# Kernel optimization log

Hardware: AMD Instinct MI355X
Metric: run time of the kernel (lower is better)

Reference implementation:

```python
import jax, jax.numpy as jnp
import numpy as np

B, N, DF = 8, 4096, 768
K1, K2, DS = 8, 2, 128
KVQ, H, ITERS = 128, 1, 3
DH = KVQ // H
EPS_SA = 1e-8
SCALE = DH ** -0.5


def layer_norm(x, g, b, eps=1e-5):
    m = jnp.mean(x, axis=-1, keepdims=True)
    v = jnp.var(x, axis=-1, keepdims=True)
    return (x - m) / jnp.sqrt(v + eps) * g + b


def gru_cell(x, h, Wih, Whh, bih, bhh):
    gi = x @ Wih.T + bih
    gh = h @ Whh.T + bhh
    ir, iz, inn = jnp.split(gi, 3, axis=-1)
    hr, hz, hn = jnp.split(gh, 3, axis=-1)
    r = jax.nn.sigmoid(ir + hr)
    z = jax.nn.sigmoid(iz + hz)
    n = jnp.tanh(inn + r * hn)
    return (1.0 - z) * n + z * h


def setup_inputs() -> dict:
    key = jax.random.key(0)
    ks = jax.random.split(key, 24)
    s = 0.02
    f32 = jnp.float32
    return {
        'tokens': jax.random.normal(ks[0], (B, N, DF), f32),
        'parent_slots': jax.random.normal(ks[1], (B, K1, DS), f32),
        'parent_masks': jax.random.uniform(ks[2], (B, K1, N), f32),
        'eps_noise': jax.random.normal(ks[3], (B, K1, K2, DS), f32),
        'ln_in_g': jnp.ones((DF,), f32), 'ln_in_b': jnp.zeros((DF,), f32),
        'ln_s_g': jnp.ones((DS,), f32), 'ln_s_b': jnp.zeros((DS,), f32),
        'Wq': jax.random.normal(ks[4], (KVQ, DS), f32) * s,
        'Wk': jax.random.normal(ks[5], (KVQ, DF), f32) * s,
        'Wv': jax.random.normal(ks[6], (KVQ, DF), f32) * s,
        'gru_Wih': jax.random.normal(ks[7], (3 * DS, KVQ), f32) * s,
        'gru_Whh': jax.random.normal(ks[8], (3 * DS, DS), f32) * s,
        'gru_bih': jnp.zeros((3 * DS,), f32),
        'gru_bhh': jnp.zeros((3 * DS,), f32),
        'mlp_ln_g': jnp.ones((DS,), f32), 'mlp_ln_b': jnp.zeros((DS,), f32),
        'mlp_W1': jax.random.normal(ks[9], (4 * DS, DS), f32) * s,
        'mlp_b1': jnp.zeros((4 * DS,), f32),
        'mlp_W2': jax.random.normal(ks[10], (DS, 4 * DS), f32) * s,
        'mlp_b2': jnp.zeros((DS,), f32),
    }


def reference(tokens, parent_slots, parent_masks, eps_noise,
              ln_in_g, ln_in_b, ln_s_g, ln_s_b, Wq, Wk, Wv,
              gru_Wih, gru_Whh, gru_bih, gru_bhh,
              mlp_ln_g, mlp_ln_b, mlp_W1, mlp_b1, mlp_W2, mlp_b2):
    BK = B * K1
    # parent-mask gating (all parents vectorized, folded into batch)
    denom = jnp.mean(parent_masks, axis=-1, keepdims=True)          # [B,K1,1]
    safe = (denom > 1e-6).astype(tokens.dtype)
    w_scaled = safe * (parent_masks / (denom + 1e-6)) + (1.0 - safe)  # [B,K1,N]
    tg = (tokens[:, None, :, :] * w_scaled[..., None]).reshape(BK, N, DF)
    slots = (parent_slots[:, :, None, :] + 0.01 * eps_noise).reshape(BK, K2, DS)

    inp = layer_norm(tg, ln_in_g, ln_in_b)
    k = (inp @ Wk.T).reshape(BK, N, H, DH)
    v = (inp @ Wv.T).reshape(BK, N, H, DH)

    attn_bw = None
    for _ in range(ITERS):
        slots_prev = slots
        sn = layer_norm(slots, ln_s_g, ln_s_b)
        q = (sn @ Wq.T).reshape(BK, K2, H, DH)
        dots = jnp.einsum('bihd,bjhd->bihj', q, k) * SCALE          # [BK,K2,H,N]
        attn = jax.nn.softmax(dots, axis=1) + EPS_SA                # softmax over slots
        attn_bw = attn
        attn_w = attn / jnp.sum(attn, axis=-1, keepdims=True)
        updates = jnp.einsum('bjhd,bihj->bihd', v, attn_w).reshape(BK * K2, KVQ)
        slots = gru_cell(updates, slots_prev.reshape(BK * K2, DS),
                         gru_Wih, gru_Whh, gru_bih, gru_bhh).reshape(BK, K2, DS)
        h = layer_norm(slots, mlp_ln_g, mlp_ln_b)
        slots = jax.nn.gelu(h @ mlp_W1.T + mlp_b1, approximate=False) @ mlp_W2.T + mlp_b2

    attn_out = jnp.mean(attn_bw, axis=2)                            # [BK,K2,N]
    child_objects = slots.reshape(B, K1 * K2, DS)
    child_gating = (attn_out.reshape(B, K1, K2, N) * parent_masks[:, :, None, :]).reshape(B, K1 * K2, N)
    return child_objects, child_gating
```

## Files before the change

### kernel.cpp

```cpp
#include <hip/hip_runtime.h>
#include <math.h>

#define SCALE_ 0.08838834764831843f

typedef __attribute__((ext_vector_type(8))) short bf16x8;
typedef __attribute__((ext_vector_type(4))) float f32x4;
typedef __attribute__((ext_vector_type(8))) unsigned short u16x8;

static const size_t OFF_VAR   = 0;
static const size_t OFF_DENOM = 32768;
static const size_t OFF_GSUM  = 32832;
static const size_t OFF_BIAS  = 33088;
static const size_t OFF_QKB   = 33344;
static const size_t OFF_SSUM  = 33472;
static const size_t OFF_SLOTS = 33600;
static const size_t OFF_Q     = 49984;
static const size_t OFF_WQBF  = 66368;
static const size_t OFF_WIHBF = 74560;
static const size_t OFF_WHHBF = 99136;
static const size_t OFF_W1BF  = 123712;
static const size_t OFF_WM2BF = 156480;
static const size_t OFF_WKVBF = 189248;
static const size_t OFF_UPART = 287552;
static const size_t OFF_KVB   = 811840;

__device__ __forceinline__ float wred64(float v) {
#pragma unroll
  for (int off = 32; off > 0; off >>= 1) v += __shfl_xor(v, off, 64);
  return v;
}

__device__ __forceinline__ unsigned short f2bf(float f) {
  unsigned u = __float_as_uint(f);
  unsigned r = (u + 0x7fffu + ((u >> 16) & 1u)) >> 16;
  return (unsigned short)r;
}

__device__ __forceinline__ unsigned pack2(float a, float b) {
  return (unsigned)f2bf(a) | ((unsigned)f2bf(b) << 16);
}

__device__ __forceinline__ float bf2f(unsigned short s) {
  return __uint_as_float((unsigned)s << 16);
}

__global__ __launch_bounds__(256) void prep_all_k(
    const float* __restrict__ Wk, const float* __restrict__ Wv,
    const float* __restrict__ g, const float* __restrict__ bb,
    const float* __restrict__ Wq, const float* __restrict__ Wih,
    const float* __restrict__ Whh, const float* __restrict__ W1,
    const float* __restrict__ W2, const float* __restrict__ pm,
    unsigned short* __restrict__ wkv, float* __restrict__ gsum,
    float* __restrict__ biasArr,
    unsigned short* __restrict__ Wqbf, unsigned short* __restrict__ Wihbf,
    unsigned short* __restrict__ Whhbf, unsigned short* __restrict__ W1bf,
    unsigned short* __restrict__ Wm2bf, float* __restrict__ denomArr)
{
  __shared__ float red4[4];
  int bi = blockIdx.x, t = threadIdx.x;
  if (bi < 64) {
    int j = bi*4 + (t >> 6), lane = t & 63;
    const float* w = (j < 128) ? (Wk + (size_t)j*768) : (Wv + (size_t)(j-128)*768);
    float gs = 0.f, bs = 0.f;
#pragma unroll
    for (int s = 0; s < 12; ++s) {
      int dd = lane + s*64;
      float wv = w[dd], gv = g[dd];
      gs += gv*wv; bs += bb[dd]*wv;
      wkv[(size_t)j*768 + dd] = f2bf(wv*gv);
    }
    gs = wred64(gs); bs = wred64(bs);
    if (lane == 0) { gsum[j] = gs; biasArr[j] = bs; }
  } else if (bi < 128) {
    int idx = (bi-64)*256 + t;  Wqbf[idx]  = f2bf(Wq[idx]);
  } else if (bi < 320) {
    int idx = (bi-128)*256 + t; Wihbf[idx] = f2bf(Wih[idx]);
  } else if (bi < 512) {
    int idx = (bi-320)*256 + t; Whhbf[idx] = f2bf(Whh[idx]);
  } else if (bi < 768) {
    int idx = (bi-512)*256 + t; W1bf[idx]  = f2bf(W1[idx]);
  } else if (bi < 1024) {
    int idx = (bi-768)*256 + t; Wm2bf[idx] = f2bf(W2[idx]);
  } else {
    int bk = bi - 1024;
    float s = 0.f;
#pragma unroll
    for (int k = 0; k < 16; ++k) s += pm[bk*4096 + t + k*256];
    s = wred64(s);
    if ((t & 63) == 0) red4[t >> 6] = s;
    __syncthreads();
    if (t == 0) denomArr[bk] = (red4[0]+red4[1]+red4[2]+red4[3])*(1.f/4096.f);
  }
}

#define DMA_B(kstep, buf) \
  { int k0_ = (kstep)*32; \
    _Pragma("unroll") \
    for (int s_ = 0; s_ < 4; ++s_) { \
      int nb_ = w*64 + s_*16; \
      __builtin_amdgcn_global_load_lds( \
        (const __attribute__((address_space(1))) void*) \
          (wkv + (size_t)(nb_ + nrow)*768 + k0_ + gsw*8), \
        (__attribute__((address_space(3))) void*)(Bs + (buf)*8192 + nb_*32), \
        16, 0, 0); \
    } }

__global__ __launch_bounds__(256) void gemm_kv_k(
    const float* __restrict__ tokens, const unsigned short* __restrict__ wkv,
    const float* __restrict__ gsum, unsigned short* __restrict__ KVb,
    float* __restrict__ varArr)
{
  __shared__ unsigned short Bs[2*8192];
  int r0 = blockIdx.x*64;
  int t = threadIdx.x;
  int w = t >> 6, lane = t & 63;
  int lm = lane & 15, lq = lane >> 4;
  int nrow = lane >> 2;
  int gsw = (lane & 3) ^ ((lane >> 3) & 3);
  int nswz = lq ^ ((lm >> 1) & 3);

  const float* aptr = tokens + (size_t)(r0 + w*16 + lm)*768 + lq*8;

  f32x4 acc[16];
#pragma unroll
  for (int c = 0; c < 16; ++c) acc[c] = f32x4{0.f, 0.f, 0.f, 0.f};
  float s1 = 0.f, s2 = 0.f;

  float4 A0[2], A1[2];
  DMA_B(0, 0);
  A0[0] = *(const float4*)(aptr);
  A1[0] = *(const float4*)(aptr + 4);
  DMA_B(1, 1);
  __builtin_amdgcn_s_waitcnt(0x0F76);
  __builtin_amdgcn_s_barrier();

#pragma unroll
  for (int k = 0; k < 24; ++k) {
    const int kb = k & 1, kn = kb ^ 1;
    float4 x0 = A0[kb], x1 = A1[kb];
    s1 += x0.x + x0.y + x0.z + x0.w + x1.x + x1.y + x1.z + x1.w;
    s2 += x0.x*x0.x + x0.y*x0.y + x0.z*x0.z + x0.w*x0.w
        + x1.x*x1.x + x1.y*x1.y + x1.z*x1.z + x1.w*x1.w;
    unsigned u0 = pack2(x0.x, x0.y), u1 = pack2(x0.z, x0.w);
    unsigned u2 = pack2(x1.x, x1.y), u3 = pack2(x1.z, x1.w);
    bf16x8 afrag;
    { uint4 tmp = make_uint4(u0, u1, u2, u3);
      afrag = *(bf16x8*)&tmp; }
    if (k < 23) {
      A0[kn] = *(const float4*)(aptr + (k+1)*32);
      A1[kn] = *(const float4*)(aptr + (k+1)*32 + 4);
    }
    const unsigned short* bsr = Bs + kb*8192;
#pragma unroll
    for (int nt = 0; nt < 16; ++nt) {
      bf16x8 bfr = *(const bf16x8*)(bsr + (nt*16 + lm)*32 + nswz*8);
      acc[nt] = __builtin_amdgcn_mfma_f32_16x16x32_bf16(afrag, bfr, acc[nt], 0, 0, 0);
    }
    if (k < 23) {
      __builtin_amdgcn_s_barrier();
      if (k < 22) {
        DMA_B(k+2, kb);
        __builtin_amdgcn_s_waitcnt(0x0F76);
      } else {
        __builtin_amdgcn_s_waitcnt(0x0F72);
      }
      __builtin_amdgcn_s_barrier();
    }
  }

  s1 += __shfl_xor(s1, 16, 64); s1 += __shfl_xor(s1, 32, 64);
  s2 += __shfl_xor(s2, 16, 64); s2 += __shfl_xor(s2, 32, 64);
  float mean = s1*(1.f/768.f);
  float var  = s2*(1.f/768.f) - mean*mean;
  if (lq == 0) varArr[r0 + w*16 + lm] = var;
  float meanR[4];
#pragma unroll
  for (int reg = 0; reg < 4; ++reg)
    meanR[reg] = __shfl(mean, lq*4 + reg, 64);
#pragma unroll
  for (int nt = 0; nt < 16; ++nt) {
    int col = nt*16 + lm;
    float gs = gsum[col];
#pragma unroll
    for (int reg = 0; reg < 4; ++reg) {
      int row = r0 + w*16 + lq*4 + reg;
      KVb[(size_t)row*256 + col] = f2bf(acc[nt][reg] - meanR[reg]*gs);
    }
  }
}

__global__ __launch_bounds__(256, 1) void slots_init_q_k(
    const float* __restrict__ ps, const float* __restrict__ eps,
    const float* __restrict__ g_s, const float* __restrict__ b_s,
    const unsigned short* __restrict__ Wqbf, const float* __restrict__ biasArr,
    float* __restrict__ slots, float* __restrict__ qg, float* __restrict__ qkb,
    float* __restrict__ Ssum)
{
  __shared__ unsigned short Fsn[2048];
  __shared__ float qkbL[16];
  int R0 = blockIdx.x*16;
  int t = threadIdx.x;
  int w = t >> 6, ln = t & 63, lm = ln & 15, lq = ln >> 4;
  if (t < 16) qkbL[t] = 0.f;
  {
    int r = t >> 4, dseg = t & 15, ds8 = dseg*8;
    int row = R0 + r, bk = row >> 1;
    float xv[8]; float s1 = 0.f, s2 = 0.f;
#pragma unroll
    for (int j = 0; j < 8; ++j) {
      int d = ds8 + j;
      float x = ps[bk*128 + d] + 0.01f*eps[row*128 + d];
      slots[row*128 + d] = x;
      xv[j] = x; s1 += x; s2 += x*x;
    }
#pragma unroll
    for (int m = 8; m >= 1; m >>= 1) {
      s1 += __shfl_xor(s1, m, 16);
      s2 += __shfl_xor(s2, m, 16);
    }
    float mean = s1*(1.f/128.f);
    float var = s2*(1.f/128.f) - mean*mean;
    float rstd = rsqrtf(var + 1e-5f);
    float sv[8];
#pragma unroll
    for (int j = 0; j < 8; ++j) {
      int d = ds8 + j;
      sv[j] = (xv[j] - mean)*rstd*g_s[d] + b_s[d];
    }
    int fa = ((dseg >> 2)*64 + (dseg & 3)*16 + r)*8;
    *(uint4*)&Fsn[fa] = make_uint4(pack2(sv[0],sv[1]), pack2(sv[2],sv[3]),
                                   pack2(sv[4],sv[5]), pack2(sv[6],sv[7]));
  }
  __syncthreads();
  {
    bf16x8 af[4];
#pragma unroll
    for (int kc = 0; kc < 4; ++kc)
      af[kc] = *(const bf16x8*)(&Fsn[(kc*64 + ln)*8]);
    float pr[4] = {0.f, 0.f, 0.f, 0.f};
#pragma unroll
    for (int i = 0; i < 2; ++i) {
      int n0 = w*32 + i*16;
      f32x4 acc = f32x4{0.f,0.f,0.f,0.f};
#pragma unroll
      for (int kc = 0; kc < 4; ++kc) {
        bf16x8 bw = *(const bf16x8*)(&Wqbf[(size_t)(n0+lm)*128 + kc*32 + lq*8]);
        acc = __builtin_amdgcn_mfma_f32_16x16x32_bf16(af[kc], bw, acc, 0,0,0);
      }
      int n = n0 + lm;
      float bk_ = biasArr[n];
#pragma unroll
      for (int reg = 0; reg < 4; ++reg) {
        int row = lq*4 + reg;
        qg[(size_t)(R0 + row)*128 + n] = acc[reg];
        pr[reg] += acc[reg]*bk_;
      }
    }
#pragma unroll
    for (int reg = 0; reg < 4; ++reg) {
#pragma unroll
      for (int m = 8; m >= 1; m >>= 1) pr[reg] += __shfl_xor(pr[reg], m, 16);
    }
    if (lm == 0) {
#pragma unroll
      for (int reg = 0; reg < 4; ++reg)
        atomicAdd(&qkbL[lq*4 + reg], pr[reg]);
    }
  }
  __syncthreads();
  if (t < 16) { qkb[R0 + t] = qkbL[t]; Ssum[R0 + t] = 0.f; }
}

__global__ __launch_bounds__(256) void attn_fused_k(
    const unsigned short* __restrict__ KVb, const float* __restrict__ qg,
    const float* __restrict__ qkb, const float* __restrict__ varArr,
    const float* __restrict__ denomArr, const float* __restrict__ pm,
    float* __restrict__ Upart, float* __restrict__ Ssum,
    float* __restrict__ outG, int last)
{
  __shared__ float KVs[32*260];
  __shared__ float qs[2048];
  __shared__ float was[16*33];
  __shared__ float qkbs[16];
  int bi = blockIdx.x;
  int b = bi & 7, ch = bi >> 3;
  int t = threadIdx.x;
#pragma unroll
  for (int s = 0; s < 2; ++s)
    ((float4*)qs)[s*256 + t] = ((const float4*)(qg + b*2048))[s*256 + t];
  if (t < 16) qkbs[t] = qkb[b*16 + t];
  int p = t >> 5, nl = t & 31;
  int iu = t >> 4, dg = t & 15;
  int bk = b*8 + p;
  float den = denomArr[bk];
  float acc8[8];
#pragma unroll
  for (int j = 0; j < 8; ++j) acc8[j] = 0.f;
  float sA0 = 0.f, sA1 = 0.f;
  const float* q0 = qs + (p*2)*128;
  const float* q1 = q0 + 128;
  __syncthreads();
  float qb0 = qkbs[p*2], qb1 = qkbs[p*2 + 1];
  for (int sub = 0; sub < 4; ++sub) {
    int n0 = ch*128 + sub*32;
    if (sub) __syncthreads();
    {
      int nn = t >> 3, jj = t & 7;
#pragma unroll
      for (int s = 0; s < 4; ++s) {
        int col8 = jj + s*8;
        u16x8 kv8 = *(const u16x8*)&KVb[((size_t)(b*4096 + n0 + nn))*256 + col8*8];
        float4 f0, f1;
        f0.x = bf2f(kv8[0]); f0.y = bf2f(kv8[1]); f0.z = bf2f(kv8[2]); f0.w = bf2f(kv8[3]);
        f1.x = bf2f(kv8[4]); f1.y = bf2f(kv8[5]); f1.z = bf2f(kv8[6]); f1.w = bf2f(kv8[7]);
        *(float4*)&KVs[nn*260 + col8*8] = f0;
        *(float4*)&KVs[nn*260 + col8*8 + 4] = f1;
      }
    }
    __syncthreads();
    float d0 = 0.f, d1 = 0.f;
    const float* kr = KVs + nl*260;
#pragma unroll 8
    for (int j4 = 0; j4 < 32; ++j4) {
      float4 kv = *(const float4*)(kr + j4*4);
      float4 qa = *(const float4*)(q0 + j4*4);
      float4 qb = *(const float4*)(q1 + j4*4);
      d0 += kv.x*qa.x + kv.y*qa.y + kv.z*qa.z + kv.w*qa.w;
      d1 += kv.x*qb.x + kv.y*qb.y + kv.z*qb.z + kv.w*qb.w;
    }
    int n = n0 + nl;
    float pmv = pm[(size_t)bk*4096 + n];
    float c = (den > 1e-6f) ? (pmv/(den + 1e-6f)) : 1.f;
    float vv = varArr[b*4096 + n];
    float al = c*rsqrtf(c*c*vv + 1e-5f);
    float dd0 = SCALE_*(al*d0 + qb0);
    float dd1 = SCALE_*(al*d1 + qb1);
    float mx = fmaxf(dd0, dd1);
    float e0 = expf(dd0 - mx), e1 = expf(dd1 - mx);
    float inv = 1.f/(e0 + e1);
    float o0 = e0*inv + 1e-8f;
    float o1 = e1*inv + 1e-8f;
    sA0 += o0; sA1 += o1;
    was[(p*2)*33 + nl] = o0*al;
    was[(p*2 + 1)*33 + nl] = o1*al;
    if (last) {
      outG[((size_t)(bk*2))*4096 + n] = o0*pmv;
      outG[((size_t)(bk*2 + 1))*4096 + n] = o1*pmv;
    }
    __syncthreads();
    const float* vb = KVs + 128 + dg*8;
    const float* wr = was + iu*33;
#pragma unroll 8
    for (int nn = 0; nn < 32; ++nn) {
      float wv = wr[nn];
      float4 v0 = *(const float4*)(vb + nn*260);
      float4 v1 = *(const float4*)(vb + nn*260 + 4);
      acc8[0] += wv*v0.x; acc8[1] += wv*v0.y; acc8[2] += wv*v0.z; acc8[3] += wv*v0.w;
      acc8[4] += wv*v1.x; acc8[5] += wv*v1.y; acc8[6] += wv*v1.z; acc8[7] += wv*v1.w;
    }
  }
#pragma unroll
  for (int m = 16; m >= 1; m >>= 1) {
    sA0 += __shfl_xor(sA0, m, 32);
    sA1 += __shfl_xor(sA1, m, 32);
  }
  if (nl == 0) {
    atomicAdd(&Ssum[bk*2], sA0);
    atomicAdd(&Ssum[bk*2 + 1], sA1);
  }
  float* up = Upart + ((size_t)(bi*16 + iu))*128 + dg*8;
  *(float4*)up = make_float4(acc8[0], acc8[1], acc8[2], acc8[3]);
  *(float4*)(up + 4) = make_float4(acc8[4], acc8[5], acc8[6], acc8[7]);
}

__global__ __launch_bounds__(256, 1) void gru_mlp_q_k(
    const float* __restrict__ Upart, const float* __restrict__ Ssum,
    const float* __restrict__ biasArr,
    const unsigned short* __restrict__ Wihbf, const unsigned short* __restrict__ Whhbf,
    const float* __restrict__ bih, const float* __restrict__ bhh,
    const float* __restrict__ mlp_g, const float* __restrict__ mlp_b,
    const unsigned short* __restrict__ W1bf, const float* __restrict__ b1,
    const unsigned short* __restrict__ Wm2bf, const float* __restrict__ b2,
    const float* __restrict__ ln_s_g, const float* __restrict__ ln_s_b,
    const unsigned short* __restrict__ Wqbf,
    float* __restrict__ slots, float* __restrict__ qg, float* __restrict__ qkb,
    float* __restrict__ SsumW, float* __restrict__ outObj, int last)
{
  __shared__ unsigned short FXx[2048], FXh[2048], Fhn[2048], Fsn[2048];
  __shared__ unsigned short Ft1[8192];
  __shared__ float G_rz[16*256];
  __shared__ float G_in[16*128];
  __shared__ float G_hn[16*128];
  __shared__ float hs_[16*128];
  __shared__ float os_[16*128];
  __shared__ float qkbL[16];

  int R0 = blockIdx.x*16;
  int t = threadIdx.x;
  int w = t >> 6, ln = t & 63;
  int lm = ln & 15, lq = ln >> 4;

  {
    int r = t >> 4, dseg = t & 15, ds8 = dseg*8;
    int R = R0 + r;
    float ua[8];
#pragma unroll
    for (int j = 0; j < 8; ++j) ua[j] = 0.f;
    const float* up = Upart + (size_t)R*128 + ds8;
#pragma unroll
    for (int ch = 0; ch < 32; ++ch) {
      float4 u0 = *(const float4*)(up + (size_t)ch*16384);
      float4 u1 = *(const float4*)(up + (size_t)ch*16384 + 4);
      ua[0]+=u0.x; ua[1]+=u0.y; ua[2]+=u0.z; ua[3]+=u0.w;
      ua[4]+=u1.x; ua[5]+=u1.y; ua[6]+=u1.z; ua[7]+=u1.w;
    }
    float Sv = 1.f/Ssum[R];
    float4 bv0 = *(const float4*)(biasArr + 128 + ds8);
    float4 bv1 = *(const float4*)(biasArr + 132 + ds8);
    float xv[8];
    xv[0]=ua[0]*Sv+bv0.x; xv[1]=ua[1]*Sv+bv0.y; xv[2]=ua[2]*Sv+bv0.z; xv[3]=ua[3]*Sv+bv0.w;
    xv[4]=ua[4]*Sv+bv1.x; xv[5]=ua[5]*Sv+bv1.y; xv[6]=ua[6]*Sv+bv1.z; xv[7]=ua[7]*Sv+bv1.w;
    float4 h0 = *(const float4*)(slots + (size_t)R*128 + ds8);
    float4 h1 = *(const float4*)(slots + (size_t)R*128 + ds8 + 4);
    *(float4*)(hs_ + r*128 + ds8) = h0;
    *(float4*)(hs_ + r*128 + ds8 + 4) = h1;
    int fa = ((dseg >> 2)*64 + (dseg & 3)*16 + r)*8;
    *(uint4*)&FXx[fa] = make_uint4(pack2(xv[0],xv[1]), pack2(xv[2],xv[3]),
                                   pack2(xv[4],xv[5]), pack2(xv[6],xv[7]));
    *(uint4*)&FXh[fa] = make_uint4(pack2(h0.x,h0.y), pack2(h0.z,h0.w),
                                   pack2(h1.x,h1.y), pack2(h1.z,h1.w));
    if (t < 16) qkbL[t] = 0.f;
  }
  __syncthreads();

  {
    bf16x8 ax[4], ah[4];
#pragma unroll
    for (int kc = 0; kc < 4; ++kc) {
      ax[kc] = *(const bf16x8*)(&FXx[(kc*64 + ln)*8]);
      ah[kc] = *(const bf16x8*)(&FXh[(kc*64 + ln)*8]);
    }
    if (w < 2) {
#pragma unroll
      for (int i = 0; i < 8; ++i) {
        int n0 = (w*8 + i)*16;
        f32x4 acc = f32x4{0.f,0.f,0.f,0.f};
#pragma unroll
        for (int kc = 0; kc < 4; ++kc) {
          bf16x8 bi_ = *(const bf16x8*)(&Wihbf[(size_t)(n0+lm)*128 + kc*32 + lq*8]);
          acc = __builtin_amdgcn_mfma_f32_16x16x32_bf16(ax[kc], bi_, acc, 0,0,0);
        }
#pragma unroll
        for (int kc = 0; kc < 4; ++kc) {
          bf16x8 bh_ = *(const bf16x8*)(&Whhbf[(size_t)(n0+lm)*128 + kc*32 + lq*8]);
          acc = __builtin_amdgcn_mfma_f32_16x16x32_bf16(ah[kc], bh_, acc, 0,0,0);
        }
#pragma unroll
        for (int reg = 0; reg < 4; ++reg)
          G_rz[(lq*4+reg)*256 + n0 + lm] = acc[reg];
      }
    } else if (w == 2) {
#pragma unroll
      for (int i = 0; i < 8; ++i) {
        int n0 = 256 + i*16;
        f32x4 acc = f32x4{0.f,0.f,0.f,0.f};
#pragma unroll
        for (int kc = 0; kc < 4; ++kc) {
          bf16x8 bi_ = *(const bf16x8*)(&Wihbf[(size_t)(n0+lm)*128 + kc*32 + lq*8]);
          acc = __builtin_amdgcn_mfma_f32_16x16x32_bf16(ax[kc], bi_, acc, 0,0,0);
        }
#pragma unroll
        for (int reg = 0; reg < 4; ++reg)
          G_in[(lq*4+reg)*128 + i*16 + lm] = acc[reg];
      }
    } else {
#pragma unroll
      for (int i = 0; i < 8; ++i) {
        int n0 = 256 + i*16;
        f32x4 acc = f32x4{0.f,0.f,0.f,0.f};
#pragma unroll
        for (int kc = 0; kc < 4; ++kc) {
          bf16x8 bh_ = *(const bf16x8*)(&Whhbf[(size_t)(n0+lm)*128 + kc*32 + lq*8]);
          acc = __builtin_amdgcn_mfma_f32_16x16x32_bf16(ah[kc], bh_, acc, 0,0,0);
        }
#pragma unroll
        for (int reg = 0; reg < 4; ++reg)
          G_hn[(lq*4+reg)*128 + i*16 + lm] = acc[reg];
      }
    }
  }
  __syncthreads();

  {
    int r = t >> 4, dseg = t & 15, ds8 = dseg*8;
    float hp[8];
    float s1 = 0.f, s2 = 0.f;
#pragma unroll
    for (int j = 0; j < 8; ++j) {
      int d = ds8 + j;
      float rg = G_rz[r*256 + d] + bih[d] + bhh[d];
      float zg = G_rz[r*256 + 128 + d] + bih[128+d] + bhh[128+d];
      float ing = G_in[r*128 + d] + bih[256+d];
      float hng = G_hn[r*128 + d] + bhh[256+d];
      float rv = 1.f/(1.f + expf(-rg));
      float zv = 1.f/(1.f + expf(-zg));
      float nv = tanhf(ing + rv*hng);
      float h0 = hs_[r*128 + d];
      float h = (1.f - zv)*nv + zv*h0;
      hp[j] = h;
      s1 += h; s2 += h*h;
    }
#pragma unroll
    for (int m = 8; m >= 1; m >>= 1) {
      s1 += __shfl_xor(s1, m, 16);
      s2 += __shfl_xor(s2, m, 16);
    }
    float mean = s1*(1.f/128.f);
    float var = s2*(1.f/128.f) - mean*mean;
    float rstd = rsqrtf(var + 1e-5f);
    float hv[8];
#pragma unroll
    for (int j = 0; j < 8; ++j) {
      int d = ds8 + j;
      hv[j] = (hp[j] - mean)*rstd*mlp_g[d] + mlp_b[d];
    }
    int fa = ((dseg >> 2)*64 + (dseg & 3)*16 + r)*8;
    *(uint4*)&Fhn[fa] = make_uint4(pack2(hv[0],hv[1]), pack2(hv[2],hv[3]),
                                   pack2(hv[4],hv[5]), pack2(hv[6],hv[7]));
  }
  __syncthreads();

  {
    bf16x8 af[4];
#pragma unroll
    for (int kc = 0; kc < 4; ++kc)
      af[kc] = *(const bf16x8*)(&Fhn[(kc*64 + ln)*8]);
#pragma unroll
    for (int i = 0; i < 8; ++i) {
      int n0 = (w*8 + i)*16;
      f32x4 acc = f32x4{0.f,0.f,0.f,0.f};
#pragma unroll
      for (int kc = 0; kc < 4; ++kc) {
        bf16x8 bw = *(const bf16x8*)(&W1bf[(size_t)(n0+lm)*128 + kc*32 + lq*8]);
        acc = __builtin_amdgcn_mfma_f32_16x16x32_bf16(af[kc], bw, acc, 0,0,0);
      }
      int kdim = n0 + lm;
      float bb = b1[kdim];
      int kc2 = kdim >> 5;
      int sub = (kdim >> 3) & 3;
      int jj = kdim & 7;
#pragma unroll
      for (int reg = 0; reg < 4; ++reg) {
        float v = acc[reg] + bb;
        float gel = 0.5f*v*(1.f + erff(v*0.70710678118654752f));
        Ft1[(kc2*64 + sub*16 + lq*4 + reg)*8 + jj] = f2bf(gel);
      }
    }
  }
  __syncthreads();

  {
#pragma unroll
    for (int i = 0; i < 2; ++i) {
      int n0 = w*32 + i*16;
      f32x4 acc = f32x4{0.f,0.f,0.f,0.f};
#pragma unroll
      for (int kc = 0; kc < 16; ++kc) {
        bf16x8 af = *(const bf16x8*)(&Ft1[(kc*64 + ln)*8]);
        bf16x8 bw = *(const bf16x8*)(&Wm2bf[(size_t)(n0+lm)*512 + kc*32 + lq*8]);
        acc = __builtin_amdgcn_mfma_f32_16x16x32_bf16(af, bw, acc, 0,0,0);
      }
      int n = n0 + lm;
      float bb = b2[n];
#pragma unroll
      for (int reg = 0; reg < 4; ++reg) {
        int row = lq*4 + reg;
        float o = acc[reg] + bb;
        slots[(size_t)(R0 + row)*128 + n] = o;
        os_[row*128 + n] = o;
        if (last) outObj[(size_t)(R0 + row)*128 + n] = o;
      }
    }
  }

  if (last) return;

  __syncthreads();
  {
    int r = t >> 4, dseg = t & 15, ds8 = dseg*8;
    float ov[8];
    float s1 = 0.f, s2 = 0.f;
#pragma unroll
    for (int j = 0; j < 8; ++j) {
      float o = os_[r*128 + ds8 + j];
      ov[j] = o; s1 += o; s2 += o*o;
    }
#pragma unroll
    for (int m = 8; m >= 1; m >>= 1) {
      s1 += __shfl_xor(s1, m, 16);
      s2 += __shfl_xor(s2, m, 16);
    }
    float mean = s1*(1.f/128.f);
    float var = s2*(1.f/128.f) - mean*mean;
    float rstd = rsqrtf(var + 1e-5f);
    float sv[8];
#pragma unroll
    for (int j = 0; j < 8; ++j) {
      int d = ds8 + j;
      sv[j] = (ov[j] - mean)*rstd*ln_s_g[d] + ln_s_b[d];
    }
    int fa = ((dseg >> 2)*64 + (dseg & 3)*16 + r)*8;
    *(uint4*)&Fsn[fa] = make_uint4(pack2(sv[0],sv[1]), pack2(sv[2],sv[3]),
                                   pack2(sv[4],sv[5]), pack2(sv[6],sv[7]));
  }
  __syncthreads();

  {
    bf16x8 af[4];
#pragma unroll
    for (int kc = 0; kc < 4; ++kc)
      af[kc] = *(const bf16x8*)(&Fsn[(kc*64 + ln)*8]);
    float pr[4] = {0.f, 0.f, 0.f, 0.f};
#pragma unroll
    for (int i = 0; i < 2; ++i) {
      int n0 = w*32 + i*16;
      f32x4 acc = f32x4{0.f,0.f,0.f,0.f};
#pragma unroll
      for (int kc = 0; kc < 4; ++kc) {
        bf16x8 bw = *(const bf16x8*)(&Wqbf[(size_t)(n0+lm)*128 + kc*32 + lq*8]);
        acc = __builtin_amdgcn_mfma_f32_16x16x32_bf16(af[kc], bw, acc, 0,0,0);
      }
      int n = n0 + lm;
      float bk_ = biasArr[n];
#pragma unroll
      for (int reg = 0; reg < 4; ++reg) {
        int row = lq*4 + reg;
        qg[(size_t)(R0 + row)*128 + n] = acc[reg];
        pr[reg] += acc[reg]*bk_;
      }
    }
#pragma unroll
    for (int reg = 0; reg < 4; ++reg) {
#pragma unroll
      for (int m = 8; m >= 1; m >>= 1) pr[reg] += __shfl_xor(pr[reg], m, 16);
    }
    if (lm == 0) {
#pragma unroll
      for (int reg = 0; reg < 4; ++reg)
        atomicAdd(&qkbL[lq*4 + reg], pr[reg]);
    }
  }
  __syncthreads();
  if (t < 16) {
    qkb[R0 + t] = qkbL[t];
    SsumW[R0 + t] = 0.f;
  }
}

extern "C" void kernel_launch(void* const* d_in, const int* in_sizes, int n_in,
                              void* d_out, int out_size, void* d_ws, size_t ws_size,
                              hipStream_t stream) {
  const float* tokens = (const float*)d_in[0];
  const float* pslots = (const float*)d_in[1];
  const float* pmasks = (const float*)d_in[2];
  const float* eps    = (const float*)d_in[3];
  const float* ln_in_g= (const float*)d_in[4];
  const float* ln_in_b= (const float*)d_in[5];
  const float* ln_s_g = (const float*)d_in[6];
  const float* ln_s_b = (const float*)d_in[7];
  const float* Wq     = (const float*)d_in[8];
  const float* Wk     = (const float*)d_in[9];
  const float* Wv     = (const float*)d_in[10];
  const float* Wih    = (const float*)d_in[11];
  const float* Whh    = (const float*)d_in[12];
  const float* bih    = (const float*)d_in[13];
  const float* bhh    = (const float*)d_in[14];
  const float* mlp_g  = (const float*)d_in[15];
  const float* mlp_b  = (const float*)d_in[16];
  const float* W1     = (const float*)d_in[17];
  const float* b1     = (const float*)d_in[18];
  const float* W2     = (const float*)d_in[19];
  const float* b2     = (const float*)d_in[20];
  float* ws  = (float*)d_ws;
  float* out = (float*)d_out;
  unsigned short* wkvbf = (unsigned short*)(ws + OFF_WKVBF);
  unsigned short* wqbf  = (unsigned short*)(ws + OFF_WQBF);
  unsigned short* wihbf = (unsigned short*)(ws + OFF_WIHBF);
  unsigned short* whhbf = (unsigned short*)(ws + OFF_WHHBF);
  unsigned short* w1bf  = (unsigned short*)(ws + OFF_W1BF);
  unsigned short* wm2bf = (unsigned short*)(ws + OFF_WM2BF);
  unsigned short* kvb   = (unsigned short*)(ws + OFF_KVB);

  prep_all_k<<<1088, 256, 0, stream>>>(Wk, Wv, ln_in_g, ln_in_b,
                                       Wq, Wih, Whh, W1, W2, pmasks,
                                       wkvbf, ws + OFF_GSUM, ws + OFF_BIAS,
                                       wqbf, wihbf, whhbf, w1bf, wm2bf,
                                       ws + OFF_DENOM);
  gemm_kv_k<<<512, 256, 0, stream>>>(tokens, wkvbf, ws + OFF_GSUM,
                                     kvb, ws + OFF_VAR);
  slots_init_q_k<<<8, 256, 0, stream>>>(pslots, eps, ln_s_g, ln_s_b,
                                        wqbf, ws + OFF_BIAS,
                                        ws + OFF_SLOTS, ws + OFF_Q,
                                        ws + OFF_QKB, ws + OFF_SSUM);
  for (int it = 0; it < 3; ++it) {
    int last = (it == 2);
    attn_fused_k<<<256, 256, 0, stream>>>(kvb, ws + OFF_Q, ws + OFF_QKB,
                                          ws + OFF_VAR, ws + OFF_DENOM, pmasks,
                                          ws + OFF_UPART, ws + OFF_SSUM,
                                          out + 16384, last);
    gru_mlp_q_k<<<8, 256, 0, stream>>>(ws + OFF_UPART, ws + OFF_SSUM,
                                       ws + OFF_BIAS, wihbf, whhbf, bih, bhh,
                                       mlp_g, mlp_b, w1bf, b1, wm2bf, b2,
                                       ln_s_g, ln_s_b, wqbf,
                                       ws + OFF_SLOTS, ws + OFF_Q, ws + OFF_QKB,
                                       ws + OFF_SSUM, out, last);
  }
}
```

Measured before the change: 380.3 us.

## Use MFMA for attention dots and updates with split K and transposed V layout

The attention kernel now computes q·k dots and the weighted V sum with bf16 MFMA instructions instead of scalar FP32 loops over LDS-staged K/V. To support this, the KV projection GEMM writes K row-major and V transposed per batch, and it loads B fragments straight from global memory into registers instead of using an LDS DMA double buffer. Each block now covers a 128-token chunk of one batch with two waves, which doubles the number of partial update buffers that the GRU kernel has to reduce. Rounding the softmax weights to bf16 adds precision loss, and the strided transposed V stores in the GEMM may cost extra write bandwidth.

```diff
diff --git a/kernel.cpp b/kernel.cpp
--- a/kernel.cpp
+++ b/kernel.cpp
@@ -5,7 +5,6 @@
 
 typedef __attribute__((ext_vector_type(8))) short bf16x8;
 typedef __attribute__((ext_vector_type(4))) float f32x4;
-typedef __attribute__((ext_vector_type(8))) unsigned short u16x8;
 
 static const size_t OFF_VAR   = 0;
 static const size_t OFF_DENOM = 32768;
@@ -22,7 +21,8 @@
 static const size_t OFF_WM2BF = 156480;
 static const size_t OFF_WKVBF = 189248;
 static const size_t OFF_UPART = 287552;
-static const size_t OFF_KVB   = 811840;
+static const size_t OFF_KB    = 1336128;
+static const size_t OFF_VT    = 3433280;
 
 __device__ __forceinline__ float wred64(float v) {
 #pragma unroll
@@ -38,10 +38,6 @@
 
 __device__ __forceinline__ unsigned pack2(float a, float b) {
   return (unsigned)f2bf(a) | ((unsigned)f2bf(b) << 16);
-}
-
-__device__ __forceinline__ float bf2f(unsigned short s) {
-  return __uint_as_float((unsigned)s << 16);
 }
 
 __global__ __launch_bounds__(256) void prep_all_k(
@@ -93,98 +89,128 @@
   }
 }
 
-#define DMA_B(kstep, buf) \
-  { int k0_ = (kstep)*32; \
-    _Pragma("unroll") \
-    for (int s_ = 0; s_ < 4; ++s_) { \
-      int nb_ = w*64 + s_*16; \
-      __builtin_amdgcn_global_load_lds( \
-        (const __attribute__((address_space(1))) void*) \
-          (wkv + (size_t)(nb_ + nrow)*768 + k0_ + gsw*8), \
-        (__attribute__((address_space(3))) void*)(Bs + (buf)*8192 + nb_*32), \
-        16, 0, 0); \
-    } }
-
 __global__ __launch_bounds__(256) void gemm_kv_k(
     const float* __restrict__ tokens, const unsigned short* __restrict__ wkv,
-    const float* __restrict__ gsum, unsigned short* __restrict__ KVb,
-    float* __restrict__ varArr)
+    const float* __restrict__ gsum, unsigned short* __restrict__ Kb,
+    unsigned short* __restrict__ VT, float* __restrict__ varArr)
 {
-  __shared__ unsigned short Bs[2*8192];
-  int r0 = blockIdx.x*64;
+  int bi = blockIdx.x;
+  int r0 = bi*64;
   int t = threadIdx.x;
-  int w = t >> 6, lane = t & 63;
-  int lm = lane & 15, lq = lane >> 4;
-  int nrow = lane >> 2;
-  int gsw = (lane & 3) ^ ((lane >> 3) & 3);
-  int nswz = lq ^ ((lm >> 1) & 3);
-
-  const float* aptr = tokens + (size_t)(r0 + w*16 + lm)*768 + lq*8;
-
-  f32x4 acc[16];
-#pragma unroll
-  for (int c = 0; c < 16; ++c) acc[c] = f32x4{0.f, 0.f, 0.f, 0.f};
-  float s1 = 0.f, s2 = 0.f;
-
-  float4 A0[2], A1[2];
-  DMA_B(0, 0);
-  A0[0] = *(const float4*)(aptr);
-  A1[0] = *(const float4*)(aptr + 4);
-  DMA_B(1, 1);
-  __builtin_amdgcn_s_waitcnt(0x0F76);
-  __builtin_amdgcn_s_barrier();
-
-#pragma unroll
+  int w = t >> 6, ln = t & 63;
+  int lm = ln & 15, lq = ln >> 4;
+  int rowbase = r0 + (w >> 1)*32;
+  int colbase = (w & 1)*128;
+
+  const float* a0p = tokens + (size_t)(rowbase + lm)*768 + lq*8;
+  const float* a1p = tokens + (size_t)(rowbase + 16 + lm)*768 + lq*8;
+  const unsigned short* bp = wkv + (size_t)(colbase + lm)*768 + lq*8;
+
+  f32x4 acc[2][8];
+#pragma unroll
+  for (int a = 0; a < 2; ++a)
+#pragma unroll
+    for (int c = 0; c < 8; ++c) acc[a][c] = f32x4{0.f, 0.f, 0.f, 0.f};
+  float s1a = 0.f, s2a = 0.f, s1b = 0.f, s2b = 0.f;
+
+  float4 cA0a = *(const float4*)(a0p);
+  float4 cA0b = *(const float4*)(a0p + 4);
+  float4 cA1a = *(const float4*)(a1p);
+  float4 cA1b = *(const float4*)(a1p + 4);
+  bf16x8 Bf[2][8];
+#pragma unroll
+  for (int nt = 0; nt < 8; ++nt)
+    Bf[0][nt] = *(const bf16x8*)(bp + (size_t)(nt*16)*768);
+
+#pragma unroll 2
   for (int k = 0; k < 24; ++k) {
-    const int kb = k & 1, kn = kb ^ 1;
-    float4 x0 = A0[kb], x1 = A1[kb];
-    s1 += x0.x + x0.y + x0.z + x0.w + x1.x + x1.y + x1.z + x1.w;
-    s2 += x0.x*x0.x + x0.y*x0.y + x0.z*x0.z + x0.w*x0.w
-        + x1.x*x1.x + x1.y*x1.y + x1.z*x1.z + x1.w*x1.w;
-    unsigned u0 = pack2(x0.x, x0.y), u1 = pack2(x0.z, x0.w);
-    unsigned u2 = pack2(x1.x, x1.y), u3 = pack2(x1.z, x1.w);
-    bf16x8 afrag;
-    { uint4 tmp = make_uint4(u0, u1, u2, u3);
-      afrag = *(bf16x8*)&tmp; }
+    const int kb = k & 1;
+    float4 nA0a, nA0b, nA1a, nA1b;
     if (k < 23) {
-      A0[kn] = *(const float4*)(aptr + (k+1)*32);
-      A1[kn] = *(const float4*)(aptr + (k+1)*32 + 4);
-    }
-    const unsigned short* bsr = Bs + kb*8192;
-#pragma unroll
-    for (int nt = 0; nt < 16; ++nt) {
-      bf16x8 bfr = *(const bf16x8*)(bsr + (nt*16 + lm)*32 + nswz*8);
-      acc[nt] = __builtin_amdgcn_mfma_f32_16x16x32_bf16(afrag, bfr, acc[nt], 0, 0, 0);
-    }
-    if (k < 23) {
-      __builtin_amdgcn_s_barrier();
-      if (k < 22) {
-        DMA_B(k+2, kb);
-        __builtin_amdgcn_s_waitcnt(0x0F76);
-      } else {
-        __builtin_amdgcn_s_waitcnt(0x0F72);
-      }
-      __builtin_amdgcn_s_barrier();
-    }
-  }
-
-  s1 += __shfl_xor(s1, 16, 64); s1 += __shfl_xor(s1, 32, 64);
-  s2 += __shfl_xor(s2, 16, 64); s2 += __shfl_xor(s2, 32, 64);
-  float mean = s1*(1.f/768.f);
-  float var  = s2*(1.f/768.f) - mean*mean;
-  if (lq == 0) varArr[r0 + w*16 + lm] = var;
-  float meanR[4];
-#pragma unroll
-  for (int reg = 0; reg < 4; ++reg)
-    meanR[reg] = __shfl(mean, lq*4 + reg, 64);
-#pragma unroll
-  for (int nt = 0; nt < 16; ++nt) {
-    int col = nt*16 + lm;
-    float gs = gsum[col];
-#pragma unroll
-    for (int reg = 0; reg < 4; ++reg) {
-      int row = r0 + w*16 + lq*4 + reg;
-      KVb[(size_t)row*256 + col] = f2bf(acc[nt][reg] - meanR[reg]*gs);
+      const float* a0n = a0p + (k+1)*32;
+      const float* a1n = a1p + (k+1)*32;
+      nA0a = *(const float4*)(a0n);
+      nA0b = *(const float4*)(a0n + 4);
+      nA1a = *(const float4*)(a1n);
+      nA1b = *(const float4*)(a1n + 4);
+#pragma unroll
+      for (int nt = 0; nt < 8; ++nt)
+        Bf[kb ^ 1][nt] = *(const bf16x8*)(bp + (size_t)(nt*16)*768 + (k+1)*32);
+    }
+    s1a += cA0a.x + cA0a.y + cA0a.z + cA0a.w + cA0b.x + cA0b.y + cA0b.z + cA0b.w;
+    s2a += cA0a.x*cA0a.x + cA0a.y*cA0a.y + cA0a.z*cA0a.z + cA0a.w*cA0a.w
+         + cA0b.x*cA0b.x + cA0b.y*cA0b.y + cA0b.z*cA0b.z + cA0b.w*cA0b.w;
+    s1b += cA1a.x + cA1a.y + cA1a.z + cA1a.w + cA1b.x + cA1b.y + cA1b.z + cA1b.w;
+    s2b += cA1a.x*cA1a.x + cA1a.y*cA1a.y + cA1a.z*cA1a.z + cA1a.w*cA1a.w
+         + cA1b.x*cA1b.x + cA1b.y*cA1b.y + cA1b.z*cA1b.z + cA1b.w*cA1b.w;
+    bf16x8 af0, af1;
+    { uint4 tmp = make_uint4(pack2(cA0a.x, cA0a.y), pack2(cA0a.z, cA0a.w),
+                             pack2(cA0b.x, cA0b.y), pack2(cA0b.z, cA0b.w));
+      af0 = *(bf16x8*)&tmp; }
+    { uint4 tmp = make_uint4(pack2(cA1a.x, cA1a.y), pack2(cA1a.z, cA1a.w),
+                             pack2(cA1b.x, cA1b.y), pack2(cA1b.z, cA1b.w));
+      af1 = *(bf16x8*)&tmp; }
+#pragma unroll
+    for (int nt = 0; nt < 8; ++nt) {
+      acc[0][nt] = __builtin_amdgcn_mfma_f32_16x16x32_bf16(af0, Bf[kb][nt], acc[0][nt], 0, 0, 0);
+      acc[1][nt] = __builtin_amdgcn_mfma_f32_16x16x32_bf16(af1, Bf[kb][nt], acc[1][nt], 0, 0, 0);
+    }
+    cA0a = nA0a; cA0b = nA0b; cA1a = nA1a; cA1b = nA1b;
+  }
+
+  s1a += __shfl_xor(s1a, 16, 64); s1a += __shfl_xor(s1a, 32, 64);
+  s2a += __shfl_xor(s2a, 16, 64); s2a += __shfl_xor(s2a, 32, 64);
+  s1b += __shfl_xor(s1b, 16, 64); s1b += __shfl_xor(s1b, 32, 64);
+  s2b += __shfl_xor(s2b, 16, 64); s2b += __shfl_xor(s2b, 32, 64);
+  float mean0 = s1a*(1.f/768.f), var0 = s2a*(1.f/768.f) - mean0*mean0;
+  float mean1 = s1b*(1.f/768.f), var1 = s2b*(1.f/768.f) - mean1*mean1;
+  if ((w & 1) == 0 && lq == 0) {
+    varArr[rowbase + lm] = var0;
+    varArr[rowbase + 16 + lm] = var1;
+  }
+  float m0R[4], m1R[4];
+#pragma unroll
+  for (int reg = 0; reg < 4; ++reg) {
+    m0R[reg] = __shfl(mean0, lq*4 + reg, 64);
+    m1R[reg] = __shfl(mean1, lq*4 + reg, 64);
+  }
+
+  if ((w & 1) == 0) {
+#pragma unroll
+    for (int nt = 0; nt < 8; ++nt) {
+      int col = nt*16 + lm;
+      float gs = gsum[col];
+#pragma unroll
+      for (int T = 0; T < 2; ++T) {
+#pragma unroll
+        for (int reg = 0; reg < 4; ++reg) {
+          int tok = rowbase + T*16 + lq*4 + reg;
+          float mv = T ? m1R[reg] : m0R[reg];
+          Kb[(size_t)tok*128 + col] = f2bf(acc[T][nt][reg] - mv*gs);
+        }
+      }
+    }
+  } else {
+#pragma unroll
+    for (int nt = 0; nt < 8; ++nt) {
+      int d = nt*16 + lm;
+      float gs = gsum[128 + d];
+#pragma unroll
+      for (int T = 0; T < 2; ++T) {
+        int tok0 = rowbase + T*16 + lq*4;
+        int b = tok0 >> 12;
+        int n = tok0 & 4095;
+        float m0 = T ? m1R[0] : m0R[0];
+        float m1 = T ? m1R[1] : m0R[1];
+        float m2 = T ? m1R[2] : m0R[2];
+        float m3 = T ? m1R[3] : m0R[3];
+        ushort4 v;
+        v.x = f2bf(acc[T][nt][0] - m0*gs);
+        v.y = f2bf(acc[T][nt][1] - m1*gs);
+        v.z = f2bf(acc[T][nt][2] - m2*gs);
+        v.w = f2bf(acc[T][nt][3] - m3*gs);
+        *(ushort4*)&VT[((size_t)(b*128 + d))*4096 + n] = v;
+      }
     }
   }
 }
@@ -271,106 +297,115 @@
   if (t < 16) { qkb[R0 + t] = qkbL[t]; Ssum[R0 + t] = 0.f; }
 }
 
-__global__ __launch_bounds__(256) void attn_fused_k(
-    const unsigned short* __restrict__ KVb, const float* __restrict__ qg,
-    const float* __restrict__ qkb, const float* __restrict__ varArr,
-    const float* __restrict__ denomArr, const float* __restrict__ pm,
+__global__ __launch_bounds__(128) void attn_fused_k(
+    const unsigned short* __restrict__ Kb, const unsigned short* __restrict__ VT,
+    const float* __restrict__ qg, const float* __restrict__ qkb,
+    const float* __restrict__ varArr, const float* __restrict__ denomArr,
+    const float* __restrict__ pm,
     float* __restrict__ Upart, float* __restrict__ Ssum,
     float* __restrict__ outG, int last)
 {
-  __shared__ float KVs[32*260];
-  __shared__ float qs[2048];
-  __shared__ float was[16*33];
-  __shared__ float qkbs[16];
+  __shared__ unsigned short Pl[2][16*68];
   int bi = blockIdx.x;
-  int b = bi & 7, ch = bi >> 3;
+  int b = bi >> 5, nch = bi & 31;
   int t = threadIdx.x;
-#pragma unroll
-  for (int s = 0; s < 2; ++s)
-    ((float4*)qs)[s*256 + t] = ((const float4*)(qg + b*2048))[s*256 + t];
-  if (t < 16) qkbs[t] = qkb[b*16 + t];
-  int p = t >> 5, nl = t & 31;
-  int iu = t >> 4, dg = t & 15;
-  int bk = b*8 + p;
-  float den = denomArr[bk];
-  float acc8[8];
-#pragma unroll
-  for (int j = 0; j < 8; ++j) acc8[j] = 0.f;
-  float sA0 = 0.f, sA1 = 0.f;
-  const float* q0 = qs + (p*2)*128;
-  const float* q1 = q0 + 128;
-  __syncthreads();
-  float qb0 = qkbs[p*2], qb1 = qkbs[p*2 + 1];
-  for (int sub = 0; sub < 4; ++sub) {
-    int n0 = ch*128 + sub*32;
-    if (sub) __syncthreads();
-    {
-      int nn = t >> 3, jj = t & 7;
-#pragma unroll
-      for (int s = 0; s < 4; ++s) {
-        int col8 = jj + s*8;
-        u16x8 kv8 = *(const u16x8*)&KVb[((size_t)(b*4096 + n0 + nn))*256 + col8*8];
-        float4 f0, f1;
-        f0.x = bf2f(kv8[0]); f0.y = bf2f(kv8[1]); f0.z = bf2f(kv8[2]); f0.w = bf2f(kv8[3]);
-        f1.x = bf2f(kv8[4]); f1.y = bf2f(kv8[5]); f1.z = bf2f(kv8[6]); f1.w = bf2f(kv8[7]);
-        *(float4*)&KVs[nn*260 + col8*8] = f0;
-        *(float4*)&KVs[nn*260 + col8*8 + 4] = f1;
-      }
-    }
-    __syncthreads();
-    float d0 = 0.f, d1 = 0.f;
-    const float* kr = KVs + nl*260;
-#pragma unroll 8
-    for (int j4 = 0; j4 < 32; ++j4) {
-      float4 kv = *(const float4*)(kr + j4*4);
-      float4 qa = *(const float4*)(q0 + j4*4);
-      float4 qb = *(const float4*)(q1 + j4*4);
-      d0 += kv.x*qa.x + kv.y*qa.y + kv.z*qa.z + kv.w*qa.w;
-      d1 += kv.x*qb.x + kv.y*qb.y + kv.z*qb.z + kv.w*qb.w;
-    }
-    int n = n0 + nl;
-    float pmv = pm[(size_t)bk*4096 + n];
-    float c = (den > 1e-6f) ? (pmv/(den + 1e-6f)) : 1.f;
-    float vv = varArr[b*4096 + n];
-    float al = c*rsqrtf(c*c*vv + 1e-5f);
-    float dd0 = SCALE_*(al*d0 + qb0);
-    float dd1 = SCALE_*(al*d1 + qb1);
-    float mx = fmaxf(dd0, dd1);
-    float e0 = expf(dd0 - mx), e1 = expf(dd1 - mx);
-    float inv = 1.f/(e0 + e1);
-    float o0 = e0*inv + 1e-8f;
-    float o1 = e1*inv + 1e-8f;
-    sA0 += o0; sA1 += o1;
-    was[(p*2)*33 + nl] = o0*al;
-    was[(p*2 + 1)*33 + nl] = o1*al;
-    if (last) {
-      outG[((size_t)(bk*2))*4096 + n] = o0*pmv;
-      outG[((size_t)(bk*2 + 1))*4096 + n] = o1*pmv;
-    }
-    __syncthreads();
-    const float* vb = KVs + 128 + dg*8;
-    const float* wr = was + iu*33;
-#pragma unroll 8
-    for (int nn = 0; nn < 32; ++nn) {
-      float wv = wr[nn];
-      float4 v0 = *(const float4*)(vb + nn*260);
-      float4 v1 = *(const float4*)(vb + nn*260 + 4);
-      acc8[0] += wv*v0.x; acc8[1] += wv*v0.y; acc8[2] += wv*v0.z; acc8[3] += wv*v0.w;
-      acc8[4] += wv*v1.x; acc8[5] += wv*v1.y; acc8[6] += wv*v1.z; acc8[7] += wv*v1.w;
-    }
-  }
-#pragma unroll
-  for (int m = 16; m >= 1; m >>= 1) {
-    sA0 += __shfl_xor(sA0, m, 32);
-    sA1 += __shfl_xor(sA1, m, 32);
-  }
-  if (nl == 0) {
-    atomicAdd(&Ssum[bk*2], sA0);
-    atomicAdd(&Ssum[bk*2 + 1], sA1);
-  }
-  float* up = Upart + ((size_t)(bi*16 + iu))*128 + dg*8;
-  *(float4*)up = make_float4(acc8[0], acc8[1], acc8[2], acc8[3]);
-  *(float4*)(up + 4) = make_float4(acc8[4], acc8[5], acc8[6], acc8[7]);
+  int wv = t >> 6, ln = t & 63;
+  int lm = ln & 15, lq = ln >> 4;
+  int ntok0 = nch*128 + wv*64;
+  unsigned short* pl = &Pl[wv][0];
+
+  bf16x8 qf[4];
+#pragma unroll
+  for (int kc = 0; kc < 4; ++kc) {
+    const float* qp = qg + (size_t)(b*16 + lm)*128 + kc*32 + lq*8;
+    float4 q0 = *(const float4*)qp;
+    float4 q1 = *(const float4*)(qp + 4);
+    uint4 tmp = make_uint4(pack2(q0.x,q0.y), pack2(q0.z,q0.w),
+                           pack2(q1.x,q1.y), pack2(q1.z,q1.w));
+    qf[kc] = *(bf16x8*)&tmp;
+  }
+  float qkbv[4];
+#pragma unroll
+  for (int reg = 0; reg < 4; ++reg) qkbv[reg] = qkb[b*16 + lq*4 + reg];
+  float den0 = denomArr[b*8 + lq*2];
+  float den1 = denomArr[b*8 + lq*2 + 1];
+  bool g0 = den0 > 1e-6f, g1 = den1 > 1e-6f;
+  float inv0 = 1.f/(den0 + 1e-6f), inv1 = 1.f/(den1 + 1e-6f);
+
+  f32x4 Uacc[8];
+#pragma unroll
+  for (int dt = 0; dt < 8; ++dt) Uacc[dt] = f32x4{0.f,0.f,0.f,0.f};
+  float sAcc[4] = {0.f, 0.f, 0.f, 0.f};
+
+#pragma unroll
+  for (int half = 0; half < 2; ++half) {
+    int tk0 = ntok0 + half*32;
+#pragma unroll
+    for (int ti = 0; ti < 2; ++ti) {
+      int n0 = tk0 + ti*16;
+      int n = n0 + lm;
+      f32x4 dacc = f32x4{0.f,0.f,0.f,0.f};
+      const unsigned short* kp = Kb + ((size_t)(b*4096 + n))*128 + lq*8;
+#pragma unroll
+      for (int kc = 0; kc < 4; ++kc) {
+        bf16x8 kf = *(const bf16x8*)(kp + kc*32);
+        dacc = __builtin_amdgcn_mfma_f32_16x16x32_bf16(qf[kc], kf, dacc, 0,0,0);
+      }
+      float vv = varArr[b*4096 + n];
+      float pm0 = pm[((size_t)(b*8 + lq*2))*4096 + n];
+      float pm1 = pm[((size_t)(b*8 + lq*2 + 1))*4096 + n];
+      float c0 = g0 ? pm0*inv0 : 1.f;
+      float c1 = g1 ? pm1*inv1 : 1.f;
+      float al0 = c0*rsqrtf(c0*c0*vv + 1e-5f);
+      float al1 = c1*rsqrtf(c1*c1*vv + 1e-5f);
+      float dd0 = SCALE_*(al0*dacc[0] + qkbv[0]);
+      float dd1 = SCALE_*(al0*dacc[1] + qkbv[1]);
+      float mx0 = fmaxf(dd0, dd1);
+      float e0 = expf(dd0 - mx0), e1 = expf(dd1 - mx0);
+      float is0 = 1.f/(e0 + e1);
+      float o0 = e0*is0 + 1e-8f, o1 = e1*is0 + 1e-8f;
+      float dd2 = SCALE_*(al1*dacc[2] + qkbv[2]);
+      float dd3 = SCALE_*(al1*dacc[3] + qkbv[3]);
+      float mx1 = fmaxf(dd2, dd3);
+      float e2 = expf(dd2 - mx1), e3 = expf(dd3 - mx1);
+      float is1 = 1.f/(e2 + e3);
+      float o2 = e2*is1 + 1e-8f, o3 = e3*is1 + 1e-8f;
+      sAcc[0] += o0; sAcc[1] += o1; sAcc[2] += o2; sAcc[3] += o3;
+      if (last) {
+        size_t ob = ((size_t)(b*16 + lq*4))*4096 + n;
+        outG[ob]          = o0*pm0;
+        outG[ob + 4096]   = o1*pm0;
+        outG[ob + 8192]   = o2*pm1;
+        outG[ob + 12288]  = o3*pm1;
+      }
+      int pc = half*32 + ti*16 + lm;
+      pl[(lq*4 + 0)*68 + pc] = f2bf(o0*al0);
+      pl[(lq*4 + 1)*68 + pc] = f2bf(o1*al0);
+      pl[(lq*4 + 2)*68 + pc] = f2bf(o2*al1);
+      pl[(lq*4 + 3)*68 + pc] = f2bf(o3*al1);
+    }
+    bf16x8 pf = *(const bf16x8*)&pl[lm*68 + half*32 + lq*8];
+    const unsigned short* vp = VT + ((size_t)(b*128 + lm))*4096 + tk0 + lq*8;
+#pragma unroll
+    for (int dt = 0; dt < 8; ++dt) {
+      bf16x8 vf = *(const bf16x8*)(vp + (size_t)(dt*16)*4096);
+      Uacc[dt] = __builtin_amdgcn_mfma_f32_16x16x32_bf16(pf, vf, Uacc[dt], 0,0,0);
+    }
+  }
+
+#pragma unroll
+  for (int reg = 0; reg < 4; ++reg) {
+    float r = sAcc[reg];
+    r += __shfl_xor(r, 1, 64); r += __shfl_xor(r, 2, 64);
+    r += __shfl_xor(r, 4, 64); r += __shfl_xor(r, 8, 64);
+    if (lm == 0) atomicAdd(&Ssum[b*16 + lq*4 + reg], r);
+  }
+  float* up = Upart + ((size_t)(b*64 + nch*2 + wv))*2048;
+#pragma unroll
+  for (int dt = 0; dt < 8; ++dt)
+#pragma unroll
+    for (int reg = 0; reg < 4; ++reg)
+      up[(lq*4 + reg)*128 + dt*16 + lm] = Uacc[dt][reg];
 }
 
 __global__ __launch_bounds__(256, 1) void gru_mlp_q_k(
@@ -406,11 +441,11 @@
     float ua[8];
 #pragma unroll
     for (int j = 0; j < 8; ++j) ua[j] = 0.f;
-    const float* up = Upart + (size_t)R*128 + ds8;
-#pragma unroll
-    for (int ch = 0; ch < 32; ++ch) {
-      float4 u0 = *(const float4*)(up + (size_t)ch*16384);
-      float4 u1 = *(const float4*)(up + (size_t)ch*16384 + 4);
+    const float* up = Upart + (size_t)blockIdx.x*131072 + r*128 + ds8;
+#pragma unroll 8
+    for (int ch = 0; ch < 64; ++ch) {
+      float4 u0 = *(const float4*)(up + (size_t)ch*2048);
+      float4 u1 = *(const float4*)(up + (size_t)ch*2048 + 4);
       ua[0]+=u0.x; ua[1]+=u0.y; ua[2]+=u0.z; ua[3]+=u0.w;
       ua[4]+=u1.x; ua[5]+=u1.y; ua[6]+=u1.z; ua[7]+=u1.w;
     }
@@ -689,7 +724,8 @@
   unsigned short* whhbf = (unsigned short*)(ws + OFF_WHHBF);
   unsigned short* w1bf  = (unsigned short*)(ws + OFF_W1BF);
   unsigned short* wm2bf = (unsigned short*)(ws + OFF_WM2BF);
-  unsigned short* kvb   = (unsigned short*)(ws + OFF_KVB);
+  unsigned short* kb    = (unsigned short*)(ws + OFF_KB);
+  unsigned short* vt    = (unsigned short*)(ws + OFF_VT);
 
   prep_all_k<<<1088, 256, 0, stream>>>(Wk, Wv, ln_in_g, ln_in_b,
                                        Wq, Wih, Whh, W1, W2, pmasks,
@@ -697,14 +733,14 @@
                                        wqbf, wihbf, whhbf, w1bf, wm2bf,
                                        ws + OFF_DENOM);
   gemm_kv_k<<<512, 256, 0, stream>>>(tokens, wkvbf, ws + OFF_GSUM,
-                                     kvb, ws + OFF_VAR);
+                                     kb, vt, ws + OFF_VAR);
   slots_init_q_k<<<8, 256, 0, stream>>>(pslots, eps, ln_s_g, ln_s_b,
                                         wqbf, ws + OFF_BIAS,
                                         ws + OFF_SLOTS, ws + OFF_Q,
                                         ws + OFF_QKB, ws + OFF_SSUM);
   for (int it = 0; it < 3; ++it) {
     int last = (it == 2);
-    attn_fused_k<<<256, 256, 0, stream>>>(kvb, ws + OFF_Q, ws + OFF_QKB,
+    attn_fused_k<<<256, 128, 0, stream>>>(kb, vt, ws + OFF_Q, ws + OFF_QKB,
                                           ws + OFF_VAR, ws + OFF_DENOM, pmasks,
                                           ws + OFF_UPART, ws + OFF_SSUM,
                                           out + 16384, last);
```

New measurement: 376.5 us. About the same (-1.0%).
